# Kernel optimization log

Measured on AMD Instinct MI355X. Metric: run time of the kernel, lower is better.

Reference implementation:

```python
import jax, jax.numpy as jnp
import numpy as np


def setup_inputs() -> dict:
    key = jax.random.key(0)
    k1, k2, k3, k4, k5 = jax.random.split(key, 5)
    B, N, E, H, D = 16, 1024, 768, 12, 64
    x = jax.random.normal(k1, (B, N, E), dtype=jnp.float32)
    W_q = jax.random.normal(k2, (H, E, D), dtype=jnp.float32)
    W_k = jax.random.normal(k3, (H, E, D), dtype=jnp.float32)
    W_v = jax.random.normal(k4, (H, E, D), dtype=jnp.float32)
    W_o = jax.random.normal(k5, (H * D, D), dtype=jnp.float32)
    return {"x": x, "W_q": W_q, "W_k": W_k, "W_v": W_v, "W_o": W_o}


def reference(x, W_q, W_k, W_v, W_o):
    # x: [B, N, E]; W_q/W_k/W_v: [H, E, D]; W_o: [H*D, D]
    B, N, E = x.shape
    H, _, D = W_q.shape
    q = jnp.einsum("bne,hed->bhnd", x, W_q)
    k = jnp.einsum("bne,hed->bhnd", x, W_k)
    v = jnp.einsum("bne,hed->bhnd", x, W_v)
    scale = 1.0 / jnp.sqrt(jnp.asarray(D, dtype=x.dtype))
    scores = jnp.einsum("bhnd,bhmd->bhnm", q, k) * scale  # [B,H,N,N]
    attn = jax.nn.softmax(scores, axis=-1)
    heads = jnp.einsum("bhnm,bhmd->bhnd", attn, v)  # [B,H,N,D]
    # concat heads along feature dim (head order preserved, like torch.concat)
    concat = jnp.transpose(heads, (0, 2, 1, 3)).reshape(B, N, H * D)
    return concat @ W_o  # [B, N, D]
```

## Files before the change

kernel.cpp:

```cpp
#include <hip/hip_runtime.h>
#include <hip/hip_bf16.h>

typedef unsigned short u16;
typedef unsigned int u32;
typedef __attribute__((ext_vector_type(8))) short bf16x8;
typedef __attribute__((ext_vector_type(4))) float f32x4;

#define DEV static __device__ __forceinline__

#define BB 16
#define NN 1024
#define EE 768
#define HH 12
#define DD 64
#define BN (BB*NN)

DEV u16 f2bf(float f){ __hip_bfloat16 h = __float2bfloat16(f); u16 u; __builtin_memcpy(&u, &h, 2); return u; }
DEV float bf2f(u16 u){ __hip_bfloat16 h; __builtin_memcpy(&h, &u, 2); return __bfloat162float(h); }
DEV void split2(float v, u16& hi, u16& lo){ hi = f2bf(v); lo = f2bf(v - bf2f(hi)); }
DEV bf16x8 ld8(const u16* p){ return *(const bf16x8*)p; }
DEV f32x4 mfma16(bf16x8 a, bf16x8 b, f32x4 c){ return __builtin_amdgcn_mfma_f32_16x16x32_bf16(a, b, c, 0, 0, 0); }
DEV float fexp2(float x){ return __builtin_amdgcn_exp2f(x); }
DEV u32 pk2(float a, float b){
  float2 f{a, b};
  __hip_bfloat162 t = __float22bfloat162_rn(f);
  u32 r; __builtin_memcpy(&r, &t, 4); return r;
}

union U8 { bf16x8 v; u16 e[8]; ushort4 q[2]; u32 w[4]; };

DEV void stage16(const u16* g, u16* l){
  __builtin_amdgcn_global_load_lds((const __attribute__((address_space(1))) void*)g,
                                   (__attribute__((address_space(3))) void*)l,
                                   16, 0, 0);
}


__global__ __launch_bounds__(256) void split_x_k(const float* __restrict__ x,
                                                 u16* __restrict__ xh, u16* __restrict__ xl){
  int i = blockIdx.x*256 + threadIdx.x;
  const float4 v = ((const float4*)x)[i];
  ushort4 h, l;
  split2(v.x, h.x, l.x);
  split2(v.y, h.y, l.y);
  split2(v.z, h.z, l.z);
  split2(v.w, h.w, l.w);
  ((ushort4*)xh)[i] = h;
  ((ushort4*)xl)[i] = l;
}

__global__ __launch_bounds__(256) void pack_bt1_k(const float* __restrict__ Wq,
                                                  const float* __restrict__ Wk,
                                                  u16* __restrict__ BT1){
  int i = blockIdx.x*256 + threadIdx.x;
  int c = i / 1536, k = i - c*1536;
  int seg = (k >= 768);
  int e = k - seg*768;
  int h = c >> 7, g = (c >> 6) & 1, d = c & 63;
  const float* W = g ? Wk : Wq;
  float v = W[((size_t)h*EE + e)*DD + d] * (g ? 1.0f : 0.125f*1.4426950408889634f);
  u16 hi, lo; split2(v, hi, lo);
  BT1[i] = seg ? lo : hi;
}

__global__ __launch_bounds__(256) void pack_bt2_k(const float* __restrict__ Wv,
                                                  u16* __restrict__ BT2){
  int i = blockIdx.x*256 + threadIdx.x;
  int c = i / 768, e = i - c*768;
  int h = c >> 6, d = c & 63;
  BT2[i] = f2bf(Wv[((size_t)h*EE + e)*DD + d]);
}

__global__ __launch_bounds__(256) void pack_wo_k(const float* __restrict__ W, u16* __restrict__ Wt){
  int i = blockIdx.x*256 + threadIdx.x;
  int j = i & 63, k = i >> 6;
  Wt[(size_t)j*EE + k] = f2bf(W[i]);
}

__global__ __launch_bounds__(256) void gemm_qk_k(const u16* __restrict__ Xh, const u16* __restrict__ Xl,
                                                 const u16* __restrict__ BT1,
                                                 u16* __restrict__ Qh, u16* __restrict__ Ql,
                                                 u16* __restrict__ Kh, u16* __restrict__ Kl){
  __shared__ u16 lds[2][4][4096];
  const int flat = blockIdx.x;
  const int swz = (flat & 7)*192 + (flat >> 3);
  const int rt = swz / 12, bc = swz - rt*12;
  const int row0 = rt*128, col0 = bc*128;
  const int tid = threadIdx.x;
  const int w = tid >> 6, l = tid & 63, lr = l & 15, lg = l >> 4;
  const int wr = w >> 1, wc = w & 1;
  const int sr = l >> 2, sce = (l & 3)*8;

  f32x4 acc[4][4];
  #pragma unroll
  for (int m=0;m<4;++m)
    #pragma unroll
    for (int n=0;n<4;++n) acc[m][n] = f32x4{0.f,0.f,0.f,0.f};

  auto stage = [&](int buf, int kt){
    const int e0 = kt*32;
    #pragma unroll
    for (int j=0;j<2;++j){
      const int r = w*32 + j*16;
      const int gr = r + sr;
      u16* dst0 = &lds[buf][0][r*32];
      u16* dst1 = &lds[buf][1][r*32];
      u16* dst2 = &lds[buf][2][r*32];
      u16* dst3 = &lds[buf][3][r*32];
      stage16(Xh  + (size_t)(row0 + gr)*EE   + e0 + sce,        dst0);
      stage16(Xl  + (size_t)(row0 + gr)*EE   + e0 + sce,        dst1);
      stage16(BT1 + (size_t)(col0 + gr)*1536 + e0 + sce,        dst2);
      stage16(BT1 + (size_t)(col0 + gr)*1536 + 768 + e0 + sce,  dst3);
    }
  };

  stage(0, 0);
  __syncthreads();

  for (int kt=0; kt<24; ++kt){
    const int buf = kt & 1;
    if (kt + 1 < 24) stage(buf ^ 1, kt + 1);

    bf16x8 ah[4], al[4], bh[4], bl[4];
    #pragma unroll
    for (int m=0;m<4;++m){
      const int off = (wr*64 + m*16 + lr)*32 + lg*8;
      ah[m] = ld8(&lds[buf][0][off]);
      al[m] = ld8(&lds[buf][1][off]);
    }
    #pragma unroll
    for (int n=0;n<4;++n){
      const int off = (wc*64 + n*16 + lr)*32 + lg*8;
      bh[n] = ld8(&lds[buf][2][off]);
      bl[n] = ld8(&lds[buf][3][off]);
    }

    __builtin_amdgcn_s_setprio(1);
    #pragma unroll
    for (int m=0;m<4;++m)
      #pragma unroll
      for (int n=0;n<4;++n){
        acc[m][n] = mfma16(ah[m], bh[n], acc[m][n]);
        acc[m][n] = mfma16(ah[m], bl[n], acc[m][n]);
        acc[m][n] = mfma16(al[m], bh[n], acc[m][n]);
      }
    __builtin_amdgcn_s_setprio(0);

    __syncthreads();
  }

  u16* Dh = wc ? Kh : Qh;
  u16* Dl = wc ? Kl : Ql;
  const size_t base = (size_t)bc*BN*DD;
  #pragma unroll
  for (int m=0;m<4;++m)
    #pragma unroll
    for (int n=0;n<4;++n)
      #pragma unroll
      for (int j=0;j<4;++j){
        int r = row0 + wr*64 + m*16 + lg*4 + j;
        int d = n*16 + lr;
        size_t o = base + (size_t)r*DD + d;
        u16 hi, lo; split2(acc[m][n][j], hi, lo);
        Dh[o] = hi; Dl[o] = lo;
      }
}

__global__ __launch_bounds__(256) void gemm_v_k(const u16* __restrict__ Xh,
                                                const u16* __restrict__ BT,
                                                u16* __restrict__ Vt){
  __shared__ u16 lds[2][2][8192];
  const int flat = blockIdx.x;
  const int swz = (flat & 7)*96 + (flat >> 3);
  const int rt = swz / 6, bc = swz - rt*6;
  const int row0 = rt*128, col0 = bc*128;
  const int tid = threadIdx.x;
  const int w = tid >> 6, l = tid & 63, lr = l & 15, lg = l >> 4;
  const int wr = w >> 1, wc = w & 1;
  const int sr = l >> 3, sce = (l & 7)*8;

  f32x4 acc[4][4];
  #pragma unroll
  for (int m=0;m<4;++m)
    #pragma unroll
    for (int n=0;n<4;++n) acc[m][n] = f32x4{0.f,0.f,0.f,0.f};

  auto stage = [&](int buf, int kt){
    const int e0 = kt*64;
    const u16* ab = Xh + (size_t)row0*EE + e0 + sce;
    const u16* bb = BT + (size_t)col0*EE + e0 + sce;
    u16* la = &lds[buf][0][0];
    u16* lb = &lds[buf][1][0];
    #pragma unroll
    for (int j=0;j<4;++j){
      const int it = j*4 + w;
      stage16(ab + (size_t)(it*8 + sr)*EE, la + it*512);
      stage16(bb + (size_t)(it*8 + sr)*EE, lb + it*512);
    }
  };

  stage(0, 0);
  __syncthreads();

  for (int kt=0; kt<12; ++kt){
    const int buf = kt & 1;
    if (kt + 1 < 12) stage(buf ^ 1, kt + 1);

    const u16* la = &lds[buf][0][0];
    const u16* lb = &lds[buf][1][0];
    bf16x8 af[4][2], bfr[4][2];
    #pragma unroll
    for (int m=0;m<4;++m)
      #pragma unroll
      for (int ks=0;ks<2;++ks)
        af[m][ks] = ld8(la + (wr*64 + m*16 + lr)*64 + ks*32 + lg*8);
    #pragma unroll
    for (int n=0;n<4;++n)
      #pragma unroll
      for (int ks=0;ks<2;++ks)
        bfr[n][ks] = ld8(lb + (wc*64 + n*16 + lr)*64 + ks*32 + lg*8);

    #pragma unroll
    for (int ks=0;ks<2;++ks)
      #pragma unroll
      for (int m=0;m<4;++m)
        #pragma unroll
        for (int n=0;n<4;++n)
          acc[m][n] = mfma16(af[m][ks], bfr[n][ks], acc[m][n]);

    __syncthreads();
  }

  #pragma unroll
  for (int m=0;m<4;++m)
    #pragma unroll
    for (int n=0;n<4;++n){
      int c = col0 + wc*64 + n*16 + lr;
      int hh = c >> 6, d = c & 63;
      int r = row0 + wr*64 + m*16 + lg*4;
      int b = r >> 10, nn = r & 1023;
      int kvb = nn & ~63, kvL = nn & 63;
      int ks = kvL >> 5, rem = kvL & 31;
      int lgp = (rem >> 2) & 3, jh = rem >> 4;
      int off = kvb + ks*32 + lgp*8 + jh*4;
      ushort4 pk;
      pk.x = f2bf(acc[m][n][0]); pk.y = f2bf(acc[m][n][1]);
      pk.z = f2bf(acc[m][n][2]); pk.w = f2bf(acc[m][n][3]);
      *(ushort4*)(Vt + ((size_t)((hh*16 + b)*DD + d))*NN + off) = pk;
    }
}

__global__ __launch_bounds__(512) void flash_k(const u16* __restrict__ Qh, const u16* __restrict__ Ql,
                                               const u16* __restrict__ Kh, const u16* __restrict__ Kl,
                                               const u16* __restrict__ Vt, u16* __restrict__ Cc){
  __shared__ u16 kbuf[2][2][4096];
  const int flat = blockIdx.x;
  const int swz = (flat & 7)*96 + (flat >> 3);
  const int qb = swz & 3, bh = swz >> 2;
  const int h = bh % 12, b = bh / 12;
  const int l = threadIdx.x & 63, w = threadIdx.x >> 6, lr = l & 15, lg = l >> 4;
  const size_t hb = (size_t)h*BN*DD + (size_t)b*NN*DD;
  const int q0 = qb*256 + w*32;

  const int srow = l >> 3;
  const int scol = 8*((l & 7) ^ srow);

  auto stage = [&](int buf, int t){
    const int kv0 = t*64;
    #pragma unroll
    for (int j=0;j<2;++j){
      const int c = w*2 + j;
      const u16* src = (c < 8) ? Kh : Kl;
      const int cr = (c & 7)*8;
      stage16(src + hb + (size_t)(kv0 + cr + srow)*DD + scol,
              &kbuf[buf][c >> 3][(c & 7)*512]);
    }
  };

  bf16x8 qfh[2][2], qfl[2][2];
  #pragma unroll
  for (int qf=0;qf<2;++qf)
    #pragma unroll
    for (int ks=0;ks<2;++ks){
      size_t o = hb + (size_t)(q0 + qf*16 + lr)*DD + ks*32 + lg*8;
      qfh[qf][ks] = ld8(Qh + o);
      qfl[qf][ks] = ld8(Ql + o);
    }

  const u16* vp[4];
  #pragma unroll
  for (int df=0;df<4;++df)
    vp[df] = Vt + ((size_t)((h*16 + b)*DD + df*16 + lr))*NN + lg*8;

  f32x4 acc[2][4];
  float mr[2] = {-1e30f,-1e30f}, ls[2] = {0.f,0.f};
  #pragma unroll
  for (int qf=0;qf<2;++qf)
    #pragma unroll
    for (int df=0;df<4;++df) acc[qf][df] = f32x4{0.f,0.f,0.f,0.f};

  stage(0, 0);
  __syncthreads();

  auto body = [&](int t, int buf){
    bf16x8 va[4][2];
    #pragma unroll
    for (int df=0;df<4;++df){
      va[df][0] = ld8(vp[df]);
      va[df][1] = ld8(vp[df] + 32);
      vp[df] += 64;
    }

    if (t + 1 < 16) stage(buf ^ 1, t + 1);

    f32x4 s[2][4];
    #pragma unroll
    for (int qf=0;qf<2;++qf)
      #pragma unroll
      for (int kf=0;kf<4;++kf) s[qf][kf] = f32x4{0.f,0.f,0.f,0.f};

    const char* kb = (const char*)&kbuf[buf][0][0];
    #pragma unroll
    for (int ks=0;ks<2;++ks){
      bf16x8 kh[4], kl2[4];
      #pragma unroll
      for (int kf=0;kf<4;++kf){
        const int r = kf*16 + lr;
        const int sw = (ks*64 + lg*16) ^ ((lr & 7) << 4);
        kh[kf]  = *(const bf16x8*)(kb + r*128 + sw);
        kl2[kf] = *(const bf16x8*)(kb + 8192 + r*128 + sw);
      }
      __builtin_amdgcn_s_setprio(1);
      #pragma unroll
      for (int qf=0;qf<2;++qf)
        #pragma unroll
        for (int kf=0;kf<4;++kf){
          s[qf][kf] = mfma16(kh[kf],  qfh[qf][ks], s[qf][kf]);
          s[qf][kf] = mfma16(kl2[kf], qfh[qf][ks], s[qf][kf]);
          s[qf][kf] = mfma16(kh[kf],  qfl[qf][ks], s[qf][kf]);
        }
      __builtin_amdgcn_s_setprio(0);
    }

    bf16x8 pb[2][2];
    #pragma unroll
    for (int qf=0;qf<2;++qf){
      float a0 = fmaxf(fmaxf(s[qf][0][0], s[qf][0][1]), fmaxf(s[qf][0][2], s[qf][0][3]));
      float a1 = fmaxf(fmaxf(s[qf][1][0], s[qf][1][1]), fmaxf(s[qf][1][2], s[qf][1][3]));
      float a2 = fmaxf(fmaxf(s[qf][2][0], s[qf][2][1]), fmaxf(s[qf][2][2], s[qf][2][3]));
      float a3 = fmaxf(fmaxf(s[qf][3][0], s[qf][3][1]), fmaxf(s[qf][3][2], s[qf][3][3]));
      float pm = fmaxf(fmaxf(a0, a1), fmaxf(a2, a3));
      if (__any(pm > mr[qf] + 8.f)){
        pm = fmaxf(pm, __shfl_xor(pm, 16, 64));
        pm = fmaxf(pm, __shfl_xor(pm, 32, 64));
        const float mn = fmaxf(mr[qf], pm);
        const float fs = fexp2(mr[qf] - mn);
        mr[qf] = mn;
        ls[qf] *= fs;
        #pragma unroll
        for (int df=0;df<4;++df)
          #pragma unroll
          for (int r=0;r<4;++r) acc[qf][df][r] *= fs;
      }
      float rs = 0.f;
      #pragma unroll
      for (int kf=0;kf<4;++kf)
        #pragma unroll
        for (int r=0;r<4;++r){
          float e = fexp2(s[qf][kf][r] - mr[qf]);
          s[qf][kf][r] = e;
          rs += e;
        }
      ls[qf] += rs;
      #pragma unroll
      for (int ks=0;ks<2;++ks){
        U8 pu;
        pu.w[0] = pk2(s[qf][2*ks][0],   s[qf][2*ks][1]);
        pu.w[1] = pk2(s[qf][2*ks][2],   s[qf][2*ks][3]);
        pu.w[2] = pk2(s[qf][2*ks+1][0], s[qf][2*ks+1][1]);
        pu.w[3] = pk2(s[qf][2*ks+1][2], s[qf][2*ks+1][3]);
        pb[qf][ks] = pu.v;
      }
    }

    __builtin_amdgcn_s_setprio(1);
    #pragma unroll
    for (int ks=0;ks<2;++ks)
      #pragma unroll
      for (int qf=0;qf<2;++qf)
        #pragma unroll
        for (int df=0;df<4;++df)
          acc[qf][df] = mfma16(va[df][ks], pb[qf][ks], acc[qf][df]);
    __builtin_amdgcn_s_setprio(0);

    __syncthreads();
  };

  for (int tt=0; tt<8; ++tt){
    body(tt*2,     0);
    body(tt*2 + 1, 1);
  }

  #pragma unroll
  for (int qf=0;qf<2;++qf){
    float t1 = ls[qf] + __shfl_xor(ls[qf], 16, 64);
    t1 += __shfl_xor(t1, 32, 64);
    const float inv = 1.0f / t1;
    #pragma unroll
    for (int df=0;df<4;++df){
      ushort4 o4;
      o4.x = f2bf(acc[qf][df][0]*inv);
      o4.y = f2bf(acc[qf][df][1]*inv);
      o4.z = f2bf(acc[qf][df][2]*inv);
      o4.w = f2bf(acc[qf][df][3]*inv);
      *(ushort4*)(Cc + (size_t)(b*NN + q0 + qf*16 + lr)*EE + h*DD + df*16 + lg*4) = o4;
    }
  }
}

__global__ __launch_bounds__(256) void gemm_o_k(const u16* __restrict__ Cc, const u16* __restrict__ Wot,
                                                float* __restrict__ out){
  __shared__ u16 lds[2][2][4096];
  const int rt = blockIdx.x;
  const int tid = threadIdx.x;
  const int w = tid >> 6, l = tid & 63, lr = l & 15, lg = l >> 4;
  const int row0 = rt*64;
  const int sr = l >> 3, sce = (l & 7)*8;

  f32x4 acc[4];
  #pragma unroll
  for (int n=0;n<4;++n) acc[n] = f32x4{0.f,0.f,0.f,0.f};

  auto stage = [&](int buf, int kt){
    const int e0 = kt*64;
    #pragma unroll
    for (int j=0;j<2;++j){
      const int r = w*16 + j*8;
      stage16(Cc  + (size_t)(row0 + r + sr)*EE + e0 + sce, &lds[buf][0][r*64]);
      stage16(Wot + (size_t)(r + sr)*EE        + e0 + sce, &lds[buf][1][r*64]);
    }
  };

  stage(0, 0);
  __syncthreads();

  for (int kt=0; kt<12; ++kt){
    const int buf = kt & 1;
    if (kt + 1 < 12) stage(buf ^ 1, kt + 1);

    bf16x8 a[2], bb[4][2];
    #pragma unroll
    for (int ks=0;ks<2;++ks)
      a[ks] = ld8(&lds[buf][0][(w*16 + lr)*64 + ks*32 + lg*8]);
    #pragma unroll
    for (int nf=0;nf<4;++nf)
      #pragma unroll
      for (int ks=0;ks<2;++ks)
        bb[nf][ks] = ld8(&lds[buf][1][(nf*16 + lr)*64 + ks*32 + lg*8]);

    #pragma unroll
    for (int ks=0;ks<2;++ks)
      #pragma unroll
      for (int nf=0;nf<4;++nf)
        acc[nf] = mfma16(a[ks], bb[nf][ks], acc[nf]);

    __syncthreads();
  }

  #pragma unroll
  for (int nf=0;nf<4;++nf)
    #pragma unroll
    for (int j=0;j<4;++j)
      out[(size_t)(row0 + w*16 + lg*4 + j)*DD + nf*16 + lr] = acc[nf][j];
}

extern "C" void kernel_launch(void* const* d_in, const int* in_sizes, int n_in,
                              void* d_out, int out_size, void* d_ws, size_t ws_size,
                              hipStream_t stream) {
  const float* x  = (const float*)d_in[0];
  const float* Wq = (const float*)d_in[1];
  const float* Wk = (const float*)d_in[2];
  const float* Wv = (const float*)d_in[3];
  const float* Wo = (const float*)d_in[4];
  float* out = (float*)d_out;

  u16* ws = (u16*)d_ws;
  const size_t SB = (size_t)12582912;
  u16* Xh  = ws;
  u16* Xl  = Xh + SB;
  u16* Qh  = Xl + SB;
  u16* Ql  = Qh + SB;
  u16* Kh  = Ql + SB;
  u16* Kl  = Kh + SB;
  u16* Vt  = Kl + SB;
  u16* Cc  = Vt + SB;
  u16* Wot = Cc + SB;
  u16* BT1 = Cc;
  u16* BT2 = Cc + 2359296;

  split_x_k <<<12288, 256, 0, stream>>>(x, Xh, Xl);
  pack_bt1_k<<<9216,  256, 0, stream>>>(Wq, Wk, BT1);
  pack_bt2_k<<<2304,  256, 0, stream>>>(Wv, BT2);
  pack_wo_k <<<192,   256, 0, stream>>>(Wo, Wot);

  gemm_qk_k<<<1536, 256, 0, stream>>>(Xh, Xl, BT1, Qh, Ql, Kh, Kl);
  gemm_v_k <<<768,  256, 0, stream>>>(Xh, BT2, Vt);
  flash_k  <<<768,  512, 0, stream>>>(Qh, Ql, Kh, Kl, Vt, Cc);
  gemm_o_k <<<256,  256, 0, stream>>>(Cc, Wot, out);
}
```

Measured before the change: 311.9 us.

## Merge prep and projection kernels; stage two K tiles per flash barrier

Folds the four pack/split kernels into one prep kernel, and merges the QK and V projection GEMMs into a single launch that dispatches on block index. This cuts launch gaps and the tail of each small grid. In flash attention it grows the K buffer to four slots, so two KV tiles are staged ahead and only one barrier is paid per two tiles. The trade-off is more LDS per block in flash, which can lower occupancy, and a shared LDS size in the merged projection kernel.

```diff
diff --git a/kernel.cpp b/kernel.cpp
--- a/kernel.cpp
+++ b/kernel.cpp
@@ -35,58 +35,55 @@
                                    16, 0, 0);
 }
 
-
-__global__ __launch_bounds__(256) void split_x_k(const float* __restrict__ x,
-                                                 u16* __restrict__ xh, u16* __restrict__ xl){
-  int i = blockIdx.x*256 + threadIdx.x;
-  const float4 v = ((const float4*)x)[i];
-  ushort4 h, l;
-  split2(v.x, h.x, l.x);
-  split2(v.y, h.y, l.y);
-  split2(v.z, h.z, l.z);
-  split2(v.w, h.w, l.w);
-  ((ushort4*)xh)[i] = h;
-  ((ushort4*)xl)[i] = l;
-}
-
-__global__ __launch_bounds__(256) void pack_bt1_k(const float* __restrict__ Wq,
-                                                  const float* __restrict__ Wk,
-                                                  u16* __restrict__ BT1){
-  int i = blockIdx.x*256 + threadIdx.x;
-  int c = i / 1536, k = i - c*1536;
-  int seg = (k >= 768);
-  int e = k - seg*768;
-  int h = c >> 7, g = (c >> 6) & 1, d = c & 63;
-  const float* W = g ? Wk : Wq;
-  float v = W[((size_t)h*EE + e)*DD + d] * (g ? 1.0f : 0.125f*1.4426950408889634f);
-  u16 hi, lo; split2(v, hi, lo);
-  BT1[i] = seg ? lo : hi;
-}
-
-__global__ __launch_bounds__(256) void pack_bt2_k(const float* __restrict__ Wv,
-                                                  u16* __restrict__ BT2){
-  int i = blockIdx.x*256 + threadIdx.x;
-  int c = i / 768, e = i - c*768;
-  int h = c >> 6, d = c & 63;
-  BT2[i] = f2bf(Wv[((size_t)h*EE + e)*DD + d]);
-}
-
-__global__ __launch_bounds__(256) void pack_wo_k(const float* __restrict__ W, u16* __restrict__ Wt){
-  int i = blockIdx.x*256 + threadIdx.x;
-  int j = i & 63, k = i >> 6;
-  Wt[(size_t)j*EE + k] = f2bf(W[i]);
-}
-
-__global__ __launch_bounds__(256) void gemm_qk_k(const u16* __restrict__ Xh, const u16* __restrict__ Xl,
-                                                 const u16* __restrict__ BT1,
-                                                 u16* __restrict__ Qh, u16* __restrict__ Ql,
-                                                 u16* __restrict__ Kh, u16* __restrict__ Kl){
-  __shared__ u16 lds[2][4][4096];
-  const int flat = blockIdx.x;
+__global__ __launch_bounds__(256) void prep_k(const float* __restrict__ x,
+                                              const float* __restrict__ Wq,
+                                              const float* __restrict__ Wk,
+                                              const float* __restrict__ Wv,
+                                              const float* __restrict__ Wo,
+                                              u16* __restrict__ Xh, u16* __restrict__ Xl,
+                                              u16* __restrict__ BT1, u16* __restrict__ BT2,
+                                              u16* __restrict__ Wot){
+  const int bid = blockIdx.x, tid = threadIdx.x;
+  if (bid < 12288){
+    int i = bid*256 + tid;
+    const float4 v = ((const float4*)x)[i];
+    ushort4 h, l;
+    split2(v.x, h.x, l.x);
+    split2(v.y, h.y, l.y);
+    split2(v.z, h.z, l.z);
+    split2(v.w, h.w, l.w);
+    ((ushort4*)Xh)[i] = h;
+    ((ushort4*)Xl)[i] = l;
+  } else if (bid < 21504){
+    int i = (bid - 12288)*256 + tid;
+    int c = i / 1536, k = i - c*1536;
+    int seg = (k >= 768);
+    int e = k - seg*768;
+    int h = c >> 7, g = (c >> 6) & 1, d = c & 63;
+    const float* W = g ? Wk : Wq;
+    float v = W[((size_t)h*EE + e)*DD + d] * (g ? 1.0f : 0.125f*1.4426950408889634f);
+    u16 hi, lo; split2(v, hi, lo);
+    BT1[i] = seg ? lo : hi;
+  } else if (bid < 23808){
+    int i = (bid - 21504)*256 + tid;
+    int c = i / 768, e = i - c*768;
+    int h = c >> 6, d = c & 63;
+    BT2[i] = f2bf(Wv[((size_t)h*EE + e)*DD + d]);
+  } else {
+    int i = (bid - 23808)*256 + tid;
+    int j = i & 63, k = i >> 6;
+    Wot[(size_t)j*EE + k] = f2bf(Wo[i]);
+  }
+}
+
+DEV void do_qk(int flat, int tid, u16* lds,
+               const u16* __restrict__ Xh, const u16* __restrict__ Xl,
+               const u16* __restrict__ BT1,
+               u16* __restrict__ Qh, u16* __restrict__ Ql,
+               u16* __restrict__ Kh, u16* __restrict__ Kl){
   const int swz = (flat & 7)*192 + (flat >> 3);
   const int rt = swz / 12, bc = swz - rt*12;
   const int row0 = rt*128, col0 = bc*128;
-  const int tid = threadIdx.x;
   const int w = tid >> 6, l = tid & 63, lr = l & 15, lg = l >> 4;
   const int wr = w >> 1, wc = w & 1;
   const int sr = l >> 2, sce = (l & 3)*8;
@@ -103,14 +100,11 @@
     for (int j=0;j<2;++j){
       const int r = w*32 + j*16;
       const int gr = r + sr;
-      u16* dst0 = &lds[buf][0][r*32];
-      u16* dst1 = &lds[buf][1][r*32];
-      u16* dst2 = &lds[buf][2][r*32];
-      u16* dst3 = &lds[buf][3][r*32];
-      stage16(Xh  + (size_t)(row0 + gr)*EE   + e0 + sce,        dst0);
-      stage16(Xl  + (size_t)(row0 + gr)*EE   + e0 + sce,        dst1);
-      stage16(BT1 + (size_t)(col0 + gr)*1536 + e0 + sce,        dst2);
-      stage16(BT1 + (size_t)(col0 + gr)*1536 + 768 + e0 + sce,  dst3);
+      u16* base = lds + buf*16384 + r*32;
+      stage16(Xh  + (size_t)(row0 + gr)*EE   + e0 + sce,        base);
+      stage16(Xl  + (size_t)(row0 + gr)*EE   + e0 + sce,        base + 4096);
+      stage16(BT1 + (size_t)(col0 + gr)*1536 + e0 + sce,        base + 8192);
+      stage16(BT1 + (size_t)(col0 + gr)*1536 + 768 + e0 + sce,  base + 12288);
     }
   };
 
@@ -124,15 +118,15 @@
     bf16x8 ah[4], al[4], bh[4], bl[4];
     #pragma unroll
     for (int m=0;m<4;++m){
-      const int off = (wr*64 + m*16 + lr)*32 + lg*8;
-      ah[m] = ld8(&lds[buf][0][off]);
-      al[m] = ld8(&lds[buf][1][off]);
+      const int off = buf*16384 + (wr*64 + m*16 + lr)*32 + lg*8;
+      ah[m] = ld8(lds + off);
+      al[m] = ld8(lds + off + 4096);
     }
     #pragma unroll
     for (int n=0;n<4;++n){
-      const int off = (wc*64 + n*16 + lr)*32 + lg*8;
-      bh[n] = ld8(&lds[buf][2][off]);
-      bl[n] = ld8(&lds[buf][3][off]);
+      const int off = buf*16384 + (wc*64 + n*16 + lr)*32 + lg*8;
+      bh[n] = ld8(lds + off + 8192);
+      bl[n] = ld8(lds + off + 12288);
     }
 
     __builtin_amdgcn_s_setprio(1);
@@ -166,15 +160,12 @@
       }
 }
 
-__global__ __launch_bounds__(256) void gemm_v_k(const u16* __restrict__ Xh,
-                                                const u16* __restrict__ BT,
-                                                u16* __restrict__ Vt){
-  __shared__ u16 lds[2][2][8192];
-  const int flat = blockIdx.x;
+DEV void do_v(int flat, int tid, u16* lds,
+              const u16* __restrict__ Xh, const u16* __restrict__ BT,
+              u16* __restrict__ Vt){
   const int swz = (flat & 7)*96 + (flat >> 3);
   const int rt = swz / 6, bc = swz - rt*6;
   const int row0 = rt*128, col0 = bc*128;
-  const int tid = threadIdx.x;
   const int w = tid >> 6, l = tid & 63, lr = l & 15, lg = l >> 4;
   const int wr = w >> 1, wc = w & 1;
   const int sr = l >> 3, sce = (l & 7)*8;
@@ -189,8 +180,8 @@
     const int e0 = kt*64;
     const u16* ab = Xh + (size_t)row0*EE + e0 + sce;
     const u16* bb = BT + (size_t)col0*EE + e0 + sce;
-    u16* la = &lds[buf][0][0];
-    u16* lb = &lds[buf][1][0];
+    u16* la = lds + buf*16384;
+    u16* lb = la + 8192;
     #pragma unroll
     for (int j=0;j<4;++j){
       const int it = j*4 + w;
@@ -206,8 +197,8 @@
     const int buf = kt & 1;
     if (kt + 1 < 12) stage(buf ^ 1, kt + 1);
 
-    const u16* la = &lds[buf][0][0];
-    const u16* lb = &lds[buf][1][0];
+    const u16* la = lds + buf*16384;
+    const u16* lb = la + 8192;
     bf16x8 af[4][2], bfr[4][2];
     #pragma unroll
     for (int m=0;m<4;++m)
@@ -250,10 +241,22 @@
     }
 }
 
+__global__ __launch_bounds__(256) void proj_k(const u16* __restrict__ Xh, const u16* __restrict__ Xl,
+                                              const u16* __restrict__ BT1, const u16* __restrict__ BT2,
+                                              u16* __restrict__ Qh, u16* __restrict__ Ql,
+                                              u16* __restrict__ Kh, u16* __restrict__ Kl,
+                                              u16* __restrict__ Vt){
+  __shared__ u16 lds[32768];
+  if (blockIdx.x < 1536)
+    do_qk(blockIdx.x, threadIdx.x, lds, Xh, Xl, BT1, Qh, Ql, Kh, Kl);
+  else
+    do_v(blockIdx.x - 1536, threadIdx.x, lds, Xh, BT2, Vt);
+}
+
 __global__ __launch_bounds__(512) void flash_k(const u16* __restrict__ Qh, const u16* __restrict__ Ql,
                                                const u16* __restrict__ Kh, const u16* __restrict__ Kl,
                                                const u16* __restrict__ Vt, u16* __restrict__ Cc){
-  __shared__ u16 kbuf[2][2][4096];
+  __shared__ u16 kbuf[4][2][4096];
   const int flat = blockIdx.x;
   const int swz = (flat & 7)*96 + (flat >> 3);
   const int qb = swz & 3, bh = swz >> 2;
@@ -299,10 +302,7 @@
     #pragma unroll
     for (int df=0;df<4;++df) acc[qf][df] = f32x4{0.f,0.f,0.f,0.f};
 
-  stage(0, 0);
-  __syncthreads();
-
-  auto body = [&](int t, int buf){
+  auto tb = [&](int buf){
     bf16x8 va[4][2];
     #pragma unroll
     for (int df=0;df<4;++df){
@@ -310,8 +310,6 @@
       va[df][1] = ld8(vp[df] + 32);
       vp[df] += 64;
     }
-
-    if (t + 1 < 16) stage(buf ^ 1, t + 1);
 
     f32x4 s[2][4];
     #pragma unroll
@@ -392,13 +390,21 @@
         for (int df=0;df<4;++df)
           acc[qf][df] = mfma16(va[df][ks], pb[qf][ks], acc[qf][df]);
     __builtin_amdgcn_s_setprio(0);
-
+  };
+
+  stage(0, 0);
+  stage(1, 1);
+  __syncthreads();
+
+  for (int ss=0; ss<8; ++ss){
+    const int cur = (ss & 1) << 1;
+    if (ss < 7){
+      stage(cur ^ 2,       2*ss + 2);
+      stage((cur ^ 2) + 1, 2*ss + 3);
+    }
+    tb(cur);
+    tb(cur + 1);
     __syncthreads();
-  };
-
-  for (int tt=0; tt<8; ++tt){
-    body(tt*2,     0);
-    body(tt*2 + 1, 1);
   }
 
   #pragma unroll
@@ -498,13 +504,8 @@
   u16* BT1 = Cc;
   u16* BT2 = Cc + 2359296;
 
-  split_x_k <<<12288, 256, 0, stream>>>(x, Xh, Xl);
-  pack_bt1_k<<<9216,  256, 0, stream>>>(Wq, Wk, BT1);
-  pack_bt2_k<<<2304,  256, 0, stream>>>(Wv, BT2);
-  pack_wo_k <<<192,   256, 0, stream>>>(Wo, Wot);
-
-  gemm_qk_k<<<1536, 256, 0, stream>>>(Xh, Xl, BT1, Qh, Ql, Kh, Kl);
-  gemm_v_k <<<768,  256, 0, stream>>>(Xh, BT2, Vt);
-  flash_k  <<<768,  512, 0, stream>>>(Qh, Ql, Kh, Kl, Vt, Cc);
-  gemm_o_k <<<256,  256, 0, stream>>>(Cc, Wot, out);
-}
+  prep_k<<<24000, 256, 0, stream>>>(x, Wq, Wk, Wv, Wo, Xh, Xl, BT1, BT2, Wot);
+  proj_k<<<2304,  256, 0, stream>>>(Xh, Xl, BT1, BT2, Qh, Ql, Kh, Kl, Vt);
+  flash_k<<<768,  512, 0, stream>>>(Qh, Ql, Kh, Kl, Vt, Cc);
+  gemm_o_k<<<256, 256, 0, stream>>>(Cc, Wot, out);
+}
```

Result: faster. 299.2 us (-4.1%).
